# Optimization experiments

Hardware: AMD Instinct MI355X
Metric: run time of the kernel (lower is better)

The kernel has to match this reference:

```python
import jax, jax.numpy as jnp
import numpy as np

B, C1, C2, H, W = 8, 256, 512, 56, 56

def setup_inputs() -> dict:
    key = jax.random.key(0)
    k1, k2, k3, k4, k5 = jax.random.split(key, 5)
    return {
        "x1": jax.random.normal(k1, (B, C1, H, W), dtype=jnp.float32),
        "x2": jax.random.normal(k2, (B, C2, H, W), dtype=jnp.float32),
        "W_proj": jax.random.normal(k3, (C1, C2), dtype=jnp.float32) * (1.0 / np.sqrt(C2)),
        "b_proj": jax.random.normal(k4, (C1,), dtype=jnp.float32) * 0.01,
        "gamma": jax.random.normal(k5, (1,), dtype=jnp.float32) * 0.1,
    }

def reference(x1, x2, W_proj, b_proj, gamma):
    b, c, h, w = x1.shape
    n = h * w
    # 1x1 conv projection C2 -> C1
    x2p = jnp.einsum('oc,bchw->bohw', W_proj, x2) + b_proj[None, :, None, None]
    query = x1.reshape(b, c, n).transpose(0, 2, 1)   # [B, N, C]
    key_ = x2p.reshape(b, c, n)                      # [B, C, N]
    value = x2p.reshape(b, c, n).transpose(0, 2, 1)  # [B, N, C]
    energy = jnp.einsum('bnc,bcm->bnm', query, key_)  # [B, N, N]
    # inverted-energy softmax: max - energy, then softmax over last dim
    energy_new = jnp.max(energy, axis=-1, keepdims=True) - energy
    attention = jax.nn.softmax(energy_new, axis=-1)
    out = jnp.einsum('bnm,bmc->bnc', attention, value)  # [B, N, C]
    out = out.transpose(0, 2, 1).reshape(b, c, h, w)
    return gamma[0] * out + x1
```

## Files before the change

### kernel.cpp

```cpp
#include <hip/hip_runtime.h>
#include <hip/hip_bf16.h>

#define C1 256
#define C2 512
#define NSP 3136
#define NT 98

typedef __attribute__((ext_vector_type(8))) short bf16x8;
typedef __attribute__((ext_vector_type(4))) float f32x4;

__device__ __forceinline__ ushort f2b(float f) {
  __hip_bfloat16 h = __float2bfloat16(f);
  return *reinterpret_cast<ushort*>(&h);
}
__device__ __forceinline__ float b2f(ushort u) {
  union { unsigned int i; float f; } v; v.i = ((unsigned int)u) << 16; return v.f;
}
__device__ __forceinline__ void gload16(const ushort* g, ushort* l) {
  __builtin_amdgcn_global_load_lds(
      (const __attribute__((address_space(1))) void*)g,
      (__attribute__((address_space(3))) void*)l, 16, 0, 0);
}
__device__ __forceinline__ void block_bar() {
  asm volatile("" ::: "memory");
  __builtin_amdgcn_s_barrier();
  asm volatile("" ::: "memory");
}

__global__ __launch_bounds__(256) void k_wtf(const float* __restrict__ W,
                                             ushort* __restrict__ Wf) {
  int ot = blockIdx.x;
  int tid = threadIdx.x;
  int lane = tid & 63, l15 = lane & 15, g = (lane >> 4) & 3;
  int cc0 = (tid >> 6) * 4;
  const float* src = W + (size_t)(ot * 16 + l15) * C2 + g * 8;
#pragma unroll
  for (int k = 0; k < 4; k++) {
    int cc = cc0 + k;
    float4 u0 = *reinterpret_cast<const float4*>(src + cc * 32);
    float4 u1 = *reinterpret_cast<const float4*>(src + cc * 32 + 4);
    bf16x8 v;
    v[0] = (short)f2b(u0.x); v[1] = (short)f2b(u0.y);
    v[2] = (short)f2b(u0.z); v[3] = (short)f2b(u0.w);
    v[4] = (short)f2b(u1.x); v[5] = (short)f2b(u1.y);
    v[6] = (short)f2b(u1.z); v[7] = (short)f2b(u1.w);
    *reinterpret_cast<bf16x8*>(Wf + ((size_t)(ot * 16 + cc)) * 512 + lane * 8) = v;
  }
}

__global__ __launch_bounds__(256) void k_x1t(const float* __restrict__ x1,
                                             ushort* __restrict__ x1t) {
  __shared__ float t[32][33];
  int b = blockIdx.z;
  int n0 = blockIdx.x * 32;
  int c0 = blockIdx.y * 32;
  int tid = threadIdx.x;
  int r = tid >> 3, q = (tid & 7) * 4;
  const float* src = x1 + ((size_t)b * C1 + (c0 + r)) * NSP + n0 + q;
  float4 v = *reinterpret_cast<const float4*>(src);
  t[r][q] = v.x; t[r][q + 1] = v.y; t[r][q + 2] = v.z; t[r][q + 3] = v.w;
  __syncthreads();
  ushort4 o;
  o.x = f2b(t[q + 0][r]); o.y = f2b(t[q + 1][r]);
  o.z = f2b(t[q + 2][r]); o.w = f2b(t[q + 3][r]);
  *reinterpret_cast<ushort4*>(x1t + ((size_t)b * NSP + n0 + r) * C1 + c0 + q) = o;
}

__global__ __launch_bounds__(256) void k_x2f(const float* __restrict__ x2,
                                             ushort* __restrict__ x2f) {
  __shared__ float t[32][33];
  int b = blockIdx.z;
  int n0 = blockIdx.x * 32;
  int cc = blockIdx.y;
  int c0 = cc * 32;
  int tid = threadIdx.x;
  int r = tid >> 3, q = (tid & 7) * 4;
  const float* src = x2 + ((size_t)b * C2 + (c0 + r)) * NSP + n0 + q;
  float4 v = *reinterpret_cast<const float4*>(src);
  t[r][q] = v.x; t[r][q + 1] = v.y; t[r][q + 2] = v.z; t[r][q + 3] = v.w;
  __syncthreads();
  int l15 = tid & 15, g = (tid >> 4) & 3, sub = tid >> 6;
  int ntl = sub & 1, ih = sub >> 1;
  int nl = ntl * 16 + l15;
  int cl = g * 8 + ih * 4;
  ushort4 o;
  o.x = f2b(t[cl + 0][nl]); o.y = f2b(t[cl + 1][nl]);
  o.z = f2b(t[cl + 2][nl]); o.w = f2b(t[cl + 3][nl]);
  int nt16 = (n0 >> 4) + ntl;
  *reinterpret_cast<ushort4*>(
      x2f + (((size_t)b * 196 + nt16) * 16 + cc) * 512 + (size_t)(tid & 63) * 8 + ih * 4) = o;
}

__global__ __launch_bounds__(256) void k_proj(const ushort* __restrict__ Wf,
    const ushort* __restrict__ x2f, const float* __restrict__ bias,
    ushort* __restrict__ Kf, ushort* __restrict__ Vf) {
  __shared__ __align__(16) ushort WL[2][8][512];
  __shared__ __align__(16) ushort XL[2][4][512];
  int bid = blockIdx.x;
  int b = bid & 7;
  int tq = bid >> 3;
  int oh = tq & 1;
  int nt = tq >> 1;
  int tid = threadIdx.x;
  int w = tid >> 6, lane = tid & 63, l15 = lane & 15, g = lane >> 4;
  int wq = w >> 1, wn = w & 1;
  int ot0 = oh * 8;
  int nt0 = nt * 4;

  auto stage = [&](int buf, int cc) {
#pragma unroll
    for (int j = 0; j < 3; j++) {
      int chunk = w * 3 + j;
      if (chunk < 8) {
        gload16(Wf + ((size_t)(ot0 + chunk) * 16 + cc) * 512 + lane * 8,
                &WL[buf][chunk][0]);
      } else {
        gload16(x2f + (((size_t)b * 196 + nt0 + (chunk - 8)) * 16 + cc) * 512 + lane * 8,
                &XL[buf][chunk - 8][0]);
      }
    }
  };

  f32x4 zero = {0.f, 0.f, 0.f, 0.f};
  f32x4 acc[4][2];
#pragma unroll
  for (int a = 0; a < 4; a++)
#pragma unroll
    for (int v = 0; v < 2; v++) acc[a][v] = zero;

  stage(0, 0);
  __syncthreads();

  for (int cc = 0; cc < 16; ++cc) {
    int cur = cc & 1;
    if (cc < 15) stage(cur ^ 1, cc + 1);
    bf16x8 A[4], Bf[2];
#pragma unroll
    for (int a = 0; a < 4; a++)
      A[a] = *reinterpret_cast<const bf16x8*>(&WL[cur][wq * 4 + a][lane * 8]);
#pragma unroll
    for (int v = 0; v < 2; v++)
      Bf[v] = *reinterpret_cast<const bf16x8*>(&XL[cur][wn * 2 + v][lane * 8]);
#pragma unroll
    for (int a = 0; a < 4; a++)
#pragma unroll
      for (int v = 0; v < 2; v++)
        acc[a][v] = __builtin_amdgcn_mfma_f32_16x16x32_bf16(A[a], Bf[v], acc[a][v], 0, 0, 0);
    __syncthreads();
  }

  int obase = oh * 128 + wq * 64;
  float4 bias4[4];
#pragma unroll
  for (int a = 0; a < 4; a++)
    bias4[a] = *reinterpret_cast<const float4*>(&bias[obase + a * 16 + g * 4]);

  int gk = (g & 1) * 4;
#pragma unroll
  for (int a = 0; a < 4; a++) {
    int laneK = (((2 * a + (g >> 1)) & 3) << 4) | l15;
    size_t oK = (size_t)(oh * 4 + wq * 2 + (a >> 1));
#pragma unroll
    for (int v = 0; v < 2; v++) {
      int nK = nt * 4 + wn * 2 + v;
      ushort4 st;
      st.x = f2b(acc[a][v][0] + bias4[a].x);
      st.y = f2b(acc[a][v][1] + bias4[a].y);
      st.z = f2b(acc[a][v][2] + bias4[a].z);
      st.w = f2b(acc[a][v][3] + bias4[a].w);
      *reinterpret_cast<ushort4*>(
          Kf + ((((size_t)b * 196 + nK) * 8 + oK) * 64 + laneK) * 8 + gk) = st;
    }
  }
  int nV = nt * 2 + wn;
#pragma unroll
  for (int v = 0; v < 2; v++) {
    int gv = ((v * 2 + (l15 >> 3)) & 3) << 4;
    int iV = l15 & 7;
#pragma unroll
    for (int a = 0; a < 4; a++) {
      int cs = oh * 8 + wq * 4 + a;
      size_t basev = ((((size_t)b * 98 + nV) * 16 + cs) * 64 + gv) * 8 + iV;
      const float* bp4 = reinterpret_cast<const float*>(&bias4[a]);
#pragma unroll
      for (int r = 0; r < 4; r++)
        Vf[basev + (size_t)(g * 4 + r) * 8] = f2b(acc[a][v][r] + bp4[r]);
    }
  }
}

__global__ __launch_bounds__(256, 3) void k_attn_s(
    const ushort* __restrict__ x1t, const ushort* __restrict__ Kf,
    const ushort* __restrict__ Vf,
    ushort* __restrict__ Po, float* __restrict__ Mv, float* __restrict__ Lv) {
  __shared__ __align__(16) ushort Kt[2][8192];
  __shared__ __align__(16) ushort Vt[8192];
  __shared__ __align__(16) ushort Plds[4][16][36];
  int bid = blockIdx.x;
  int x = bid & 7;
  int j = bid >> 3;
  int s = (4802 * j) / 96;
  int e = (4802 * (j + 1)) / 96;
  int tid = threadIdx.x;
  int w = tid >> 6;
  int lane = tid & 63;
  int l15 = lane & 15;
  int g = lane >> 4;
  int nloc = w * 16 + g * 4;

  const ushort* kg = Kf + (size_t)x * 196 * 8 * 512;
  const ushort* vg = Vf + (size_t)x * 98 * 16 * 512;
  int soff = w * 2048;

  f32x4 zero = {0.f, 0.f, 0.f, 0.f};
  f32x4 O[16];
  f32x4 O17 = zero;
  float M[4];
  bf16x8 qf[8];
  bf16x8 onesf;
#pragma unroll
  for (int i = 0; i < 8; i++) onesf[i] = (short)0x3F80;

  auto resetacc = [&]() {
#pragma unroll
    for (int i = 0; i < 16; i++) O[i] = zero;
    O17 = zero;
#pragma unroll
    for (int r = 0; r < 4; r++) M[r] = -3.0e38f;
  };
  auto loadQ = [&](int u) {
    const ushort* qb = x1t + ((size_t)x * NSP + u * 64 + w * 16 + l15) * C1 + g * 8;
#pragma unroll
    for (int cc = 0; cc < 8; cc++)
      qf[cc] = *reinterpret_cast<const bf16x8*>(qb + cc * 32);
  };

  int u = s / 98;
  int kv = s - u * 98;
  loadQ(u);
  resetacc();
  {
    const ushort* ks = kg + (size_t)kv * 8192 + soff + lane * 8;
#pragma unroll
    for (int jj = 0; jj < 4; ++jj) gload16(ks + jj * 512, &Kt[0][soff] + jj * 512);
  }
  asm volatile("s_waitcnt vmcnt(0)" ::: "memory");
  block_bar();

  int cur = 0;
  for (int i = s; i < e; ++i) {
    {
      const ushort* vs = vg + (size_t)kv * 8192 + soff + lane * 8;
#pragma unroll
      for (int jj = 0; jj < 4; ++jj) gload16(vs + jj * 512, &Vt[soff] + jj * 512);
    }
    asm volatile("" ::: "memory");
    if (i + 1 < e) {
      int kvn = (kv == 97) ? 0 : kv + 1;
      const ushort* ks = kg + (size_t)kvn * 8192 + soff + lane * 8;
#pragma unroll
      for (int jj = 0; jj < 4; ++jj) gload16(ks + jj * 512, &Kt[cur ^ 1][soff] + jj * 512);
    }
    asm volatile("" ::: "memory");

    f32x4 s0a = zero, s0b = zero, s1a = zero, s1b = zero;
    const ushort* kb = &Kt[cur][0];
    __builtin_amdgcn_s_setprio(1);
#pragma unroll
    for (int cc = 0; cc < 8; cc += 2) {
      bf16x8 k00 = *reinterpret_cast<const bf16x8*>(kb + ((size_t)cc * 64 + lane) * 8);
      bf16x8 k10 = *reinterpret_cast<const bf16x8*>(kb + ((size_t)(8 + cc) * 64 + lane) * 8);
      bf16x8 k01 = *reinterpret_cast<const bf16x8*>(kb + ((size_t)(cc + 1) * 64 + lane) * 8);
      bf16x8 k11 = *reinterpret_cast<const bf16x8*>(kb + ((size_t)(9 + cc) * 64 + lane) * 8);
      s0a = __builtin_amdgcn_mfma_f32_16x16x32_bf16(qf[cc], k00, s0a, 0, 0, 0);
      s1a = __builtin_amdgcn_mfma_f32_16x16x32_bf16(qf[cc], k10, s1a, 0, 0, 0);
      s0b = __builtin_amdgcn_mfma_f32_16x16x32_bf16(qf[cc + 1], k01, s0b, 0, 0, 0);
      s1b = __builtin_amdgcn_mfma_f32_16x16x32_bf16(qf[cc + 1], k11, s1b, 0, 0, 0);
    }
    __builtin_amdgcn_s_setprio(0);

    float a0[4], a1[4], tmax[4];
#pragma unroll
    for (int r = 0; r < 4; r++) {
      a0[r] = -(s0a[r] + s0b[r]);
      a1[r] = -(s1a[r] + s1b[r]);
      float mx = fmaxf(a0[r], a1[r]);
      mx = fmaxf(mx, __shfl_xor(mx, 1));
      mx = fmaxf(mx, __shfl_xor(mx, 2));
      mx = fmaxf(mx, __shfl_xor(mx, 4));
      mx = fmaxf(mx, __shfl_xor(mx, 8));
      tmax[r] = mx;
    }
    float d01 = fmaxf(tmax[0] - M[0], tmax[1] - M[1]);
    float d23 = fmaxf(tmax[2] - M[2], tmax[3] - M[3]);
    if (__any(fmaxf(d01, d23) > 3.0f)) {
      float scv[4];
#pragma unroll
      for (int r = 0; r < 4; r++) {
        float nm = fmaxf(M[r], tmax[r]);
        scv[r] = __expf(M[r] - nm);
        M[r] = nm;
      }
#pragma unroll
      for (int i2 = 0; i2 < 16; i2++) {
#pragma unroll
        for (int r = 0; r < 4; r++) O[i2][r] *= scv[r];
      }
#pragma unroll
      for (int r = 0; r < 4; r++) O17[r] *= scv[r];
    }
#pragma unroll
    for (int r = 0; r < 4; r++) {
      float p0 = __expf(a0[r] - M[r]);
      float p1 = __expf(a1[r] - M[r]);
      Plds[w][g * 4 + r][l15] = f2b(p0);
      Plds[w][g * 4 + r][16 + l15] = f2b(p1);
    }

    if (i + 1 < e) { asm volatile("s_waitcnt vmcnt(4)" ::: "memory"); }
    else           { asm volatile("s_waitcnt vmcnt(0)" ::: "memory"); }
    block_bar();

    asm volatile("s_waitcnt lgkmcnt(0)" ::: "memory");
    bf16x8 pf = *reinterpret_cast<const bf16x8*>(&Plds[w][l15][g * 8]);
    __builtin_amdgcn_s_setprio(1);
#pragma unroll
    for (int cs = 0; cs < 16; ++cs) {
      bf16x8 vf = *reinterpret_cast<const bf16x8*>(&Vt[0] + ((size_t)cs * 64 + lane) * 8);
      O[cs] = __builtin_amdgcn_mfma_f32_16x16x32_bf16(pf, vf, O[cs], 0, 0, 0);
    }
    O17 = __builtin_amdgcn_mfma_f32_16x16x32_bf16(pf, onesf, O17, 0, 0, 0);
    __builtin_amdgcn_s_setprio(0);

    asm volatile("s_waitcnt vmcnt(0)" ::: "memory");
    block_bar();
    cur ^= 1;

    if ((i + 1 == e) || (kv == 97)) {
      int firstj = (9408 * u + 95) / 4802;
      int slot = (x * 49 + u) * 3 + (j - firstj);
#pragma unroll
      for (int cs = 0; cs < 16; cs++) {
        int c = cs * 16 + l15;
        ushort4 st;
        st.x = f2b(O[cs][0]); st.y = f2b(O[cs][1]);
        st.z = f2b(O[cs][2]); st.w = f2b(O[cs][3]);
        *reinterpret_cast<ushort4*>(Po + ((size_t)slot * 256 + c) * 64 + nloc) = st;
      }
      if (l15 == 0) {
#pragma unroll
        for (int r = 0; r < 4; r++) {
          Mv[(size_t)slot * 64 + nloc + r] = M[r];
          Lv[(size_t)slot * 64 + nloc + r] = O17[r];
        }
      }
      if (i + 1 < e && kv == 97) { u += 1; loadQ(u); resetacc(); }
    }
    kv = (kv == 97) ? 0 : kv + 1;
  }
}

__global__ __launch_bounds__(256) void k_comb3(
    const ushort* __restrict__ Po, const float* __restrict__ Mv,
    const float* __restrict__ Lv, const float* __restrict__ x1,
    const float* __restrict__ gamma, float* __restrict__ out) {
  int bid = blockIdx.x;
  int x = bid & 7;
  int u = bid >> 3;
  int tid = threadIdx.x;
  int n = tid & 63;
  int c0 = (tid >> 6) * 64;
  int firstj = (9408 * u + 95) / 4802;
  int lastj = (96 * (98 * u + 97) + 95) / 4802;
  int np = lastj - firstj + 1;
  size_t base = (size_t)(x * 49 + u) * 3;
  bool has2 = (np >= 3);

  float M0 = Mv[(base + 0) * 64 + n];
  float M1 = Mv[(base + 1) * 64 + n];
  float M2 = has2 ? Mv[(base + 2) * 64 + n] : -3.0e38f;
  float L0 = Lv[(base + 0) * 64 + n];
  float L1 = Lv[(base + 1) * 64 + n];
  float L2 = has2 ? Lv[(base + 2) * 64 + n] : 0.f;
  float Mg = fmaxf(fmaxf(M0, M1), M2);
  float w0 = __expf(M0 - Mg), w1 = __expf(M1 - Mg);
  float w2 = has2 ? __expf(M2 - Mg) : 0.f;
  float rl = gamma[0] / (w0 * L0 + w1 * L1 + w2 * L2);

  const ushort* p0 = Po + ((base + 0) * 256) * 64 + n;
  const ushort* p1 = Po + ((base + 1) * 256) * 64 + n;
  const ushort* p2 = Po + ((base + 2) * 256) * 64 + n;
  size_t ob = (size_t)x * C1 * NSP + u * 64 + n;
#pragma unroll 4
  for (int c = c0; c < c0 + 64; ++c) {
    float acc = w0 * b2f(p0[(size_t)c * 64]) + w1 * b2f(p1[(size_t)c * 64]);
    if (has2) acc += w2 * b2f(p2[(size_t)c * 64]);
    size_t idx = ob + (size_t)c * NSP;
    out[idx] = acc * rl + x1[idx];
  }
}

template<int SPLIT>
__global__ __launch_bounds__(256, 3) void k_attn(
    const ushort* __restrict__ x1t, const ushort* __restrict__ Kf,
    const ushort* __restrict__ Vf, const float* __restrict__ x1,
    const float* __restrict__ gamma, float* __restrict__ out,
    ushort* __restrict__ Po, float* __restrict__ Mv, float* __restrict__ Lv) {
  __shared__ __align__(16) ushort Kt[2][8192];
  __shared__ __align__(16) ushort Vt[8192];
  __shared__ __align__(16) ushort Plds[4][16][36];
  int bid = blockIdx.x;
  int b = bid & 7;
  int qt = SPLIT ? (bid >> 4) : (bid >> 3);
  int h = SPLIT ? ((bid >> 3) & 1) : 0;
  int t0 = h * 49;
  int t1 = SPLIT ? (t0 + 49) : NT;
  int tid = threadIdx.x;
  int w = tid >> 6;
  int lane = tid & 63;
  int l15 = lane & 15;
  int g = lane >> 4;
  int n0 = qt * 64 + w * 16;

  bf16x8 qf[8];
  const ushort* qb = x1t + ((size_t)b * NSP + n0 + l15) * C1 + g * 8;
#pragma unroll
  for (int cc = 0; cc < 8; cc++)
    qf[cc] = *reinterpret_cast<const bf16x8*>(qb + cc * 32);

  f32x4 zero = {0.f, 0.f, 0.f, 0.f};
  f32x4 O[16];
#pragma unroll
  for (int i = 0; i < 16; i++) O[i] = zero;
  f32x4 O17 = zero;
  float M[4];
#pragma unroll
  for (int r = 0; r < 4; r++) M[r] = -3.0e38f;
  bf16x8 onesf;
#pragma unroll
  for (int i = 0; i < 8; i++) onesf[i] = (short)0x3F80;

  const ushort* kg = Kf + (size_t)b * 196 * 8 * 512;
  const ushort* vg = Vf + (size_t)b * 98 * 16 * 512;
  int soff = w * 2048;

  {
    const ushort* ks = kg + (size_t)t0 * 8192 + soff + lane * 8;
#pragma unroll
    for (int jj = 0; jj < 4; ++jj) gload16(ks + jj * 512, &Kt[0][soff] + jj * 512);
  }
  asm volatile("s_waitcnt vmcnt(0)" ::: "memory");
  block_bar();

  int cur = 0;
  for (int t = t0; t < t1; ++t) {
    {
      const ushort* vs = vg + (size_t)t * 8192 + soff + lane * 8;
#pragma unroll
      for (int jj = 0; jj < 4; ++jj) gload16(vs + jj * 512, &Vt[soff] + jj * 512);
    }
    asm volatile("" ::: "memory");
    if (t + 1 < t1) {
      const ushort* ks = kg + (size_t)(t + 1) * 8192 + soff + lane * 8;
#pragma unroll
      for (int jj = 0; jj < 4; ++jj) gload16(ks + jj * 512, &Kt[cur ^ 1][soff] + jj * 512);
    }
    asm volatile("" ::: "memory");

    f32x4 s0a = zero, s0b = zero, s1a = zero, s1b = zero;
    const ushort* kb = &Kt[cur][0];
    __builtin_amdgcn_s_setprio(1);
#pragma unroll
    for (int cc = 0; cc < 8; cc += 2) {
      bf16x8 k00 = *reinterpret_cast<const bf16x8*>(kb + ((size_t)cc * 64 + lane) * 8);
      bf16x8 k10 = *reinterpret_cast<const bf16x8*>(kb + ((size_t)(8 + cc) * 64 + lane) * 8);
      bf16x8 k01 = *reinterpret_cast<const bf16x8*>(kb + ((size_t)(cc + 1) * 64 + lane) * 8);
      bf16x8 k11 = *reinterpret_cast<const bf16x8*>(kb + ((size_t)(9 + cc) * 64 + lane) * 8);
      s0a = __builtin_amdgcn_mfma_f32_16x16x32_bf16(qf[cc], k00, s0a, 0, 0, 0);
      s1a = __builtin_amdgcn_mfma_f32_16x16x32_bf16(qf[cc], k10, s1a, 0, 0, 0);
      s0b = __builtin_amdgcn_mfma_f32_16x16x32_bf16(qf[cc + 1], k01, s0b, 0, 0, 0);
      s1b = __builtin_amdgcn_mfma_f32_16x16x32_bf16(qf[cc + 1], k11, s1b, 0, 0, 0);
    }
    __builtin_amdgcn_s_setprio(0);

    float a0[4], a1[4], tmax[4];
#pragma unroll
    for (int r = 0; r < 4; r++) {
      a0[r] = -(s0a[r] + s0b[r]);
      a1[r] = -(s1a[r] + s1b[r]);
      float mx = fmaxf(a0[r], a1[r]);
      mx = fmaxf(mx, __shfl_xor(mx, 1));
      mx = fmaxf(mx, __shfl_xor(mx, 2));
      mx = fmaxf(mx, __shfl_xor(mx, 4));
      mx = fmaxf(mx, __shfl_xor(mx, 8));
      tmax[r] = mx;
    }
    float d01 = fmaxf(tmax[0] - M[0], tmax[1] - M[1]);
    float d23 = fmaxf(tmax[2] - M[2], tmax[3] - M[3]);
    if (__any(fmaxf(d01, d23) > 3.0f)) {
      float scv[4];
#pragma unroll
      for (int r = 0; r < 4; r++) {
        float nm = fmaxf(M[r], tmax[r]);
        scv[r] = __expf(M[r] - nm);
        M[r] = nm;
      }
#pragma unroll
      for (int i = 0; i < 16; i++) {
#pragma unroll
        for (int r = 0; r < 4; r++) O[i][r] *= scv[r];
      }
#pragma unroll
      for (int r = 0; r < 4; r++) O17[r] *= scv[r];
    }
#pragma unroll
    for (int r = 0; r < 4; r++) {
      float p0 = __expf(a0[r] - M[r]);
      float p1 = __expf(a1[r] - M[r]);
      Plds[w][g * 4 + r][l15] = f2b(p0);
      Plds[w][g * 4 + r][16 + l15] = f2b(p1);
    }

    if (t + 1 < t1) { asm volatile("s_waitcnt vmcnt(4)" ::: "memory"); }
    else            { asm volatile("s_waitcnt vmcnt(0)" ::: "memory"); }
    block_bar();

    asm volatile("s_waitcnt lgkmcnt(0)" ::: "memory");
    bf16x8 pf = *reinterpret_cast<const bf16x8*>(&Plds[w][l15][g * 8]);
    __builtin_amdgcn_s_setprio(1);
#pragma unroll
    for (int cs = 0; cs < 16; ++cs) {
      bf16x8 vf = *reinterpret_cast<const bf16x8*>(&Vt[0] + ((size_t)cs * 64 + lane) * 8);
      O[cs] = __builtin_amdgcn_mfma_f32_16x16x32_bf16(pf, vf, O[cs], 0, 0, 0);
    }
    O17 = __builtin_amdgcn_mfma_f32_16x16x32_bf16(pf, onesf, O17, 0, 0, 0);
    __builtin_amdgcn_s_setprio(0);

    asm volatile("s_waitcnt vmcnt(0)" ::: "memory");
    block_bar();
    cur ^= 1;
  }

  if (SPLIT) {
    int pb = bid;
    int nloc = w * 16 + g * 4;
#pragma unroll
    for (int cs = 0; cs < 16; cs++) {
      int c = cs * 16 + l15;
      ushort4 st;
      st.x = f2b(O[cs][0]); st.y = f2b(O[cs][1]);
      st.z = f2b(O[cs][2]); st.w = f2b(O[cs][3]);
      *reinterpret_cast<ushort4*>(Po + ((size_t)pb * 256 + c) * 64 + nloc) = st;
    }
    if (l15 == 0) {
#pragma unroll
      for (int r = 0; r < 4; r++) {
        Mv[(size_t)pb * 64 + nloc + r] = M[r];
        Lv[(size_t)pb * 64 + nloc + r] = O17[r];
      }
    }
  } else {
    float gm = gamma[0];
    float rl[4];
#pragma unroll
    for (int r = 0; r < 4; r++) rl[r] = gm / O17[r];
    size_t ob = (size_t)b * C1 * NSP + n0 + (size_t)g * 4;
#pragma unroll
    for (int cs = 0; cs < 16; cs++) {
      size_t idx = ob + (size_t)(cs * 16 + l15) * NSP;
      float4 x4 = *reinterpret_cast<const float4*>(&x1[idx]);
      float4 o4;
      o4.x = O[cs][0] * rl[0] + x4.x;
      o4.y = O[cs][1] * rl[1] + x4.y;
      o4.z = O[cs][2] * rl[2] + x4.z;
      o4.w = O[cs][3] * rl[3] + x4.w;
      *reinterpret_cast<float4*>(&out[idx]) = o4;
    }
  }
}

__global__ __launch_bounds__(256) void k_comb(
    const ushort* __restrict__ Po, const float* __restrict__ Mv,
    const float* __restrict__ Lv, const float* __restrict__ x1,
    const float* __restrict__ gamma, float* __restrict__ out) {
  int bid = blockIdx.x;
  int b = bid & 7;
  int qt = bid >> 3;
  int tid = threadIdx.x;
  int n = tid & 63;
  int c0 = (tid >> 6) * 64;
  int pb0 = qt * 16 + b;
  int pb1 = qt * 16 + 8 + b;
  int n0 = qt * 64;
  float M0 = Mv[(size_t)pb0 * 64 + n], M1 = Mv[(size_t)pb1 * 64 + n];
  float L0 = Lv[(size_t)pb0 * 64 + n], L1 = Lv[(size_t)pb1 * 64 + n];
  float Ms = fmaxf(M0, M1);
  float w0 = __expf(M0 - Ms), w1 = __expf(M1 - Ms);
  float rl = gamma[0] / (w0 * L0 + w1 * L1);
  const ushort* p0 = Po + (size_t)pb0 * 16384 + n;
  const ushort* p1 = Po + (size_t)pb1 * 16384 + n;
#pragma unroll 4
  for (int c = c0; c < c0 + 64; ++c) {
    float o0 = b2f(p0[(size_t)c * 64]);
    float o1 = b2f(p1[(size_t)c * 64]);
    size_t idx = ((size_t)b * C1 + c) * NSP + n0 + n;
    out[idx] = (w0 * o0 + w1 * o1) * rl + x1[idx];
  }
}

extern "C" void kernel_launch(void* const* d_in, const int* in_sizes, int n_in,
                              void* d_out, int out_size, void* d_ws, size_t ws_size,
                              hipStream_t stream) {
  const float* x1 = (const float*)d_in[0];
  const float* x2 = (const float*)d_in[1];
  const float* W = (const float*)d_in[2];
  const float* bp = (const float*)d_in[3];
  const float* gamma = (const float*)d_in[4];
  float* out = (float*)d_out;

  char* ws = (char*)d_ws;
  ushort* Wf = (ushort*)(ws + 0);
  ushort* x1t = (ushort*)(ws + 262144);
  ushort* Kf = (ushort*)(ws + 13107200);
  ushort* Vf = (ushort*)(ws + 25952256);
  ushort* Po = (ushort*)(ws + 38797312);
  float* Mv = (float*)(ws + 77332480);
  float* Lv = (float*)(ws + 77633536);
  ushort* Pof = (ushort*)(ws + 38797312);
  float* Mvf = (float*)(ws + 64487424);
  float* Lvf = (float*)(ws + 64688128);
  ushort* x2f = (ushort*)d_out;

  k_wtf<<<dim3(16), dim3(256), 0, stream>>>(W, Wf);
  k_x1t<<<dim3(98, 8, 8), dim3(256), 0, stream>>>(x1, x1t);
  k_x2f<<<dim3(98, 16, 8), dim3(256), 0, stream>>>(x2, x2f);
  k_proj<<<dim3(784), dim3(256), 0, stream>>>(Wf, x2f, bp, Kf, Vf);

  if (ws_size >= 77934592ULL) {
    k_attn_s<<<dim3(768), dim3(256), 0, stream>>>(x1t, Kf, Vf, Po, Mv, Lv);
    k_comb3<<<dim3(392), dim3(256), 0, stream>>>(Po, Mv, Lv, x1, gamma, out);
  } else if (ws_size >= 64888832ULL) {
    k_attn<1><<<dim3(784), dim3(256), 0, stream>>>(x1t, Kf, Vf, x1, gamma, out,
                                                   Pof, Mvf, Lvf);
    k_comb<<<dim3(392), dim3(256), 0, stream>>>(Pof, Mvf, Lvf, x1, gamma, out);
  } else {
    k_attn<0><<<dim3(392), dim3(256), 0, stream>>>(x1t, Kf, Vf, x1, gamma, out,
                                                   Pof, Mvf, Lvf);
  }
}
```

Before: 241.8 us.

## Add 8-wave attention kernel with 128-row query tiles and stream-K split

```diff
diff --git a/kernel.cpp b/kernel.cpp
--- a/kernel.cpp
+++ b/kernel.cpp
@@ -189,6 +189,221 @@
   }
 }
 
+__global__ __launch_bounds__(512, 4) void k_attn_w8(
+    const ushort* __restrict__ x1t, const ushort* __restrict__ Kf,
+    const ushort* __restrict__ Vf,
+    ushort* __restrict__ Po, float* __restrict__ Mv, float* __restrict__ Lv) {
+  __shared__ __align__(16) ushort Kt[2][8192];
+  __shared__ __align__(16) ushort Vt[2][8192];
+  __shared__ __align__(16) ushort Plds[8][16][36];
+  int bid = blockIdx.x;
+  int x = bid & 7;
+  int j = bid >> 3;
+  int s = (2450 * j) / 64;
+  int e = (2450 * (j + 1)) / 64;
+  int tid = threadIdx.x;
+  int w = tid >> 6;
+  int lane = tid & 63;
+  int l15 = lane & 15;
+  int g = lane >> 4;
+  int nloc = w * 16 + g * 4;
+
+  const ushort* kg = Kf + (size_t)x * 196 * 8 * 512;
+  const ushort* vg = Vf + (size_t)x * 98 * 16 * 512;
+  int soff = w * 1024;
+
+  f32x4 zero = {0.f, 0.f, 0.f, 0.f};
+  f32x4 O[16];
+  f32x4 O17 = zero;
+  float M[4];
+  bf16x8 qf[8];
+  bf16x8 onesf;
+#pragma unroll
+  for (int i = 0; i < 8; i++) onesf[i] = (short)0x3F80;
+
+  auto resetacc = [&]() {
+#pragma unroll
+    for (int i = 0; i < 16; i++) O[i] = zero;
+    O17 = zero;
+#pragma unroll
+    for (int r = 0; r < 4; r++) M[r] = -3.0e38f;
+  };
+  auto loadQ = [&](int u) {
+    int qrow = u * 128 + w * 16;
+    if (qrow >= NSP) qrow = 0;
+    const ushort* qb = x1t + ((size_t)x * NSP + qrow + l15) * C1 + g * 8;
+#pragma unroll
+    for (int cc = 0; cc < 8; cc++)
+      qf[cc] = *reinterpret_cast<const bf16x8*>(qb + cc * 32);
+  };
+  auto stageK = [&](int buf, int t) {
+    const ushort* ks = kg + (size_t)t * 8192 + soff + lane * 8;
+    gload16(ks, &Kt[buf][soff]);
+    gload16(ks + 512, &Kt[buf][soff + 512]);
+  };
+  auto stageV = [&](int buf, int t) {
+    const ushort* vs = vg + (size_t)t * 8192 + soff + lane * 8;
+    gload16(vs, &Vt[buf][soff]);
+    gload16(vs + 512, &Vt[buf][soff + 512]);
+  };
+
+  int u = s / 98;
+  int kv = s - u * 98;
+  loadQ(u);
+  resetacc();
+  stageK(0, kv);
+  stageV(0, kv);
+
+  int cur = 0;
+  for (int i = s; i < e; ++i) {
+    asm volatile("s_waitcnt vmcnt(2)" ::: "memory");
+    block_bar();
+    if (i + 1 < e) {
+      int kvn = (kv == 97) ? 0 : kv + 1;
+      stageK(cur ^ 1, kvn);
+      stageV(cur ^ 1, kvn);
+    }
+
+    f32x4 s0a = zero, s0b = zero, s1a = zero, s1b = zero;
+    const ushort* kb = &Kt[cur][0];
+    __builtin_amdgcn_s_setprio(1);
+#pragma unroll
+    for (int cc = 0; cc < 8; cc += 2) {
+      bf16x8 k00 = *reinterpret_cast<const bf16x8*>(kb + ((size_t)cc * 64 + lane) * 8);
+      bf16x8 k10 = *reinterpret_cast<const bf16x8*>(kb + ((size_t)(8 + cc) * 64 + lane) * 8);
+      bf16x8 k01 = *reinterpret_cast<const bf16x8*>(kb + ((size_t)(cc + 1) * 64 + lane) * 8);
+      bf16x8 k11 = *reinterpret_cast<const bf16x8*>(kb + ((size_t)(9 + cc) * 64 + lane) * 8);
+      s0a = __builtin_amdgcn_mfma_f32_16x16x32_bf16(qf[cc], k00, s0a, 0, 0, 0);
+      s1a = __builtin_amdgcn_mfma_f32_16x16x32_bf16(qf[cc], k10, s1a, 0, 0, 0);
+      s0b = __builtin_amdgcn_mfma_f32_16x16x32_bf16(qf[cc + 1], k01, s0b, 0, 0, 0);
+      s1b = __builtin_amdgcn_mfma_f32_16x16x32_bf16(qf[cc + 1], k11, s1b, 0, 0, 0);
+    }
+    __builtin_amdgcn_s_setprio(0);
+
+    float a0[4], a1[4], tmax[4];
+#pragma unroll
+    for (int r = 0; r < 4; r++) {
+      a0[r] = -(s0a[r] + s0b[r]);
+      a1[r] = -(s1a[r] + s1b[r]);
+      float mx = fmaxf(a0[r], a1[r]);
+      mx = fmaxf(mx, __shfl_xor(mx, 1));
+      mx = fmaxf(mx, __shfl_xor(mx, 2));
+      mx = fmaxf(mx, __shfl_xor(mx, 4));
+      mx = fmaxf(mx, __shfl_xor(mx, 8));
+      tmax[r] = mx;
+    }
+    float d01 = fmaxf(tmax[0] - M[0], tmax[1] - M[1]);
+    float d23 = fmaxf(tmax[2] - M[2], tmax[3] - M[3]);
+    if (__any(fmaxf(d01, d23) > 3.0f)) {
+      float scv[4];
+#pragma unroll
+      for (int r = 0; r < 4; r++) {
+        float nm = fmaxf(M[r], tmax[r]);
+        scv[r] = __expf(M[r] - nm);
+        M[r] = nm;
+      }
+#pragma unroll
+      for (int i2 = 0; i2 < 16; i2++) {
+#pragma unroll
+        for (int r = 0; r < 4; r++) O[i2][r] *= scv[r];
+      }
+#pragma unroll
+      for (int r = 0; r < 4; r++) O17[r] *= scv[r];
+    }
+#pragma unroll
+    for (int r = 0; r < 4; r++) {
+      Plds[w][g * 4 + r][l15] = f2b(__expf(a0[r] - M[r]));
+      Plds[w][g * 4 + r][16 + l15] = f2b(__expf(a1[r] - M[r]));
+    }
+
+    if (i + 1 < e) { asm volatile("s_waitcnt vmcnt(4)" ::: "memory"); }
+    else           { asm volatile("s_waitcnt vmcnt(0)" ::: "memory"); }
+    block_bar();
+
+    asm volatile("s_waitcnt lgkmcnt(0)" ::: "memory");
+    bf16x8 pf = *reinterpret_cast<const bf16x8*>(&Plds[w][l15][g * 8]);
+    const ushort* vb = &Vt[cur][0];
+    __builtin_amdgcn_s_setprio(1);
+#pragma unroll
+    for (int cs = 0; cs < 16; ++cs) {
+      bf16x8 vf = *reinterpret_cast<const bf16x8*>(vb + ((size_t)cs * 64 + lane) * 8);
+      O[cs] = __builtin_amdgcn_mfma_f32_16x16x32_bf16(pf, vf, O[cs], 0, 0, 0);
+    }
+    O17 = __builtin_amdgcn_mfma_f32_16x16x32_bf16(pf, onesf, O17, 0, 0, 0);
+    __builtin_amdgcn_s_setprio(0);
+    cur ^= 1;
+
+    if ((i + 1 == e) || (kv == 97)) {
+      if (u * 128 + w * 16 < NSP) {
+        int firstj = (6272 * u + 63) / 2450;
+        int slot = (x * 25 + u) * 4 + (j - firstj);
+#pragma unroll
+        for (int cs = 0; cs < 16; cs++) {
+          int c = cs * 16 + l15;
+          ushort4 st;
+          st.x = f2b(O[cs][0]); st.y = f2b(O[cs][1]);
+          st.z = f2b(O[cs][2]); st.w = f2b(O[cs][3]);
+          *reinterpret_cast<ushort4*>(Po + ((size_t)slot * 256 + c) * 128 + nloc) = st;
+        }
+        if (l15 == 0) {
+#pragma unroll
+          for (int r = 0; r < 4; r++) {
+            Mv[(size_t)slot * 128 + nloc + r] = M[r];
+            Lv[(size_t)slot * 128 + nloc + r] = O17[r];
+          }
+        }
+      }
+      if (i + 1 < e && kv == 97) { u += 1; loadQ(u); resetacc(); }
+    }
+    kv = (kv == 97) ? 0 : kv + 1;
+  }
+}
+
+__global__ __launch_bounds__(256) void k_comb4w(
+    const ushort* __restrict__ Po, const float* __restrict__ Mv,
+    const float* __restrict__ Lv, const float* __restrict__ x1,
+    const float* __restrict__ gamma, float* __restrict__ out) {
+  int bid = blockIdx.x;
+  int x = bid & 7;
+  int u = bid >> 3;
+  int tid = threadIdx.x;
+  int n = tid & 127;
+  int c0 = (tid >> 7) * 128;
+  if (u * 128 + n >= NSP) return;
+  int firstj = (6272 * u + 63) / 2450;
+  int lastj = (6272 * u + 6271) / 2450;
+  int np = lastj - firstj + 1;
+  size_t base = (size_t)(x * 25 + u) * 4;
+
+  float Mp[4], Lp[4], wq[4];
+  float Mg = -3.0e38f;
+#pragma unroll
+  for (int q = 0; q < 4; q++) {
+    if (q < np) {
+      Mp[q] = Mv[(base + q) * 128 + n];
+      Lp[q] = Lv[(base + q) * 128 + n];
+      Mg = fmaxf(Mg, Mp[q]);
+    }
+  }
+  float Ls = 0.f;
+#pragma unroll
+  for (int q = 0; q < 4; q++) {
+    wq[q] = (q < np) ? __expf(Mp[q] - Mg) : 0.f;
+    if (q < np) Ls += wq[q] * Lp[q];
+  }
+  float rl = gamma[0] / Ls;
+  size_t ob = (size_t)x * C1 * NSP + (size_t)u * 128 + n;
+#pragma unroll 2
+  for (int c = c0; c < c0 + 128; ++c) {
+    float acc = 0.f;
+#pragma unroll
+    for (int q = 0; q < 4; q++)
+      if (q < np) acc += wq[q] * b2f(Po[((base + q) * 256 + c) * 128 + n]);
+    size_t idx = ob + (size_t)c * NSP;
+    out[idx] = acc * rl + x1[idx];
+  }
+}
+
 __global__ __launch_bounds__(256, 3) void k_attn_s(
     const ushort* __restrict__ x1t, const ushort* __restrict__ Kf,
     const ushort* __restrict__ Vf,
@@ -311,10 +526,8 @@
     }
 #pragma unroll
     for (int r = 0; r < 4; r++) {
-      float p0 = __expf(a0[r] - M[r]);
-      float p1 = __expf(a1[r] - M[r]);
-      Plds[w][g * 4 + r][l15] = f2b(p0);
-      Plds[w][g * 4 + r][16 + l15] = f2b(p1);
+      Plds[w][g * 4 + r][l15] = f2b(__expf(a0[r] - M[r]));
+      Plds[w][g * 4 + r][16 + l15] = f2b(__expf(a1[r] - M[r]));
     }
 
     if (i + 1 < e) { asm volatile("s_waitcnt vmcnt(4)" ::: "memory"); }
@@ -400,214 +613,6 @@
   }
 }
 
-template<int SPLIT>
-__global__ __launch_bounds__(256, 3) void k_attn(
-    const ushort* __restrict__ x1t, const ushort* __restrict__ Kf,
-    const ushort* __restrict__ Vf, const float* __restrict__ x1,
-    const float* __restrict__ gamma, float* __restrict__ out,
-    ushort* __restrict__ Po, float* __restrict__ Mv, float* __restrict__ Lv) {
-  __shared__ __align__(16) ushort Kt[2][8192];
-  __shared__ __align__(16) ushort Vt[8192];
-  __shared__ __align__(16) ushort Plds[4][16][36];
-  int bid = blockIdx.x;
-  int b = bid & 7;
-  int qt = SPLIT ? (bid >> 4) : (bid >> 3);
-  int h = SPLIT ? ((bid >> 3) & 1) : 0;
-  int t0 = h * 49;
-  int t1 = SPLIT ? (t0 + 49) : NT;
-  int tid = threadIdx.x;
-  int w = tid >> 6;
-  int lane = tid & 63;
-  int l15 = lane & 15;
-  int g = lane >> 4;
-  int n0 = qt * 64 + w * 16;
-
-  bf16x8 qf[8];
-  const ushort* qb = x1t + ((size_t)b * NSP + n0 + l15) * C1 + g * 8;
-#pragma unroll
-  for (int cc = 0; cc < 8; cc++)
-    qf[cc] = *reinterpret_cast<const bf16x8*>(qb + cc * 32);
-
-  f32x4 zero = {0.f, 0.f, 0.f, 0.f};
-  f32x4 O[16];
-#pragma unroll
-  for (int i = 0; i < 16; i++) O[i] = zero;
-  f32x4 O17 = zero;
-  float M[4];
-#pragma unroll
-  for (int r = 0; r < 4; r++) M[r] = -3.0e38f;
-  bf16x8 onesf;
-#pragma unroll
-  for (int i = 0; i < 8; i++) onesf[i] = (short)0x3F80;
-
-  const ushort* kg = Kf + (size_t)b * 196 * 8 * 512;
-  const ushort* vg = Vf + (size_t)b * 98 * 16 * 512;
-  int soff = w * 2048;
-
-  {
-    const ushort* ks = kg + (size_t)t0 * 8192 + soff + lane * 8;
-#pragma unroll
-    for (int jj = 0; jj < 4; ++jj) gload16(ks + jj * 512, &Kt[0][soff] + jj * 512);
-  }
-  asm volatile("s_waitcnt vmcnt(0)" ::: "memory");
-  block_bar();
-
-  int cur = 0;
-  for (int t = t0; t < t1; ++t) {
-    {
-      const ushort* vs = vg + (size_t)t * 8192 + soff + lane * 8;
-#pragma unroll
-      for (int jj = 0; jj < 4; ++jj) gload16(vs + jj * 512, &Vt[soff] + jj * 512);
-    }
-    asm volatile("" ::: "memory");
-    if (t + 1 < t1) {
-      const ushort* ks = kg + (size_t)(t + 1) * 8192 + soff + lane * 8;
-#pragma unroll
-      for (int jj = 0; jj < 4; ++jj) gload16(ks + jj * 512, &Kt[cur ^ 1][soff] + jj * 512);
-    }
-    asm volatile("" ::: "memory");
-
-    f32x4 s0a = zero, s0b = zero, s1a = zero, s1b = zero;
-    const ushort* kb = &Kt[cur][0];
-    __builtin_amdgcn_s_setprio(1);
-#pragma unroll
-    for (int cc = 0; cc < 8; cc += 2) {
-      bf16x8 k00 = *reinterpret_cast<const bf16x8*>(kb + ((size_t)cc * 64 + lane) * 8);
-      bf16x8 k10 = *reinterpret_cast<const bf16x8*>(kb + ((size_t)(8 + cc) * 64 + lane) * 8);
-      bf16x8 k01 = *reinterpret_cast<const bf16x8*>(kb + ((size_t)(cc + 1) * 64 + lane) * 8);
-      bf16x8 k11 = *reinterpret_cast<const bf16x8*>(kb + ((size_t)(9 + cc) * 64 + lane) * 8);
-      s0a = __builtin_amdgcn_mfma_f32_16x16x32_bf16(qf[cc], k00, s0a, 0, 0, 0);
-      s1a = __builtin_amdgcn_mfma_f32_16x16x32_bf16(qf[cc], k10, s1a, 0, 0, 0);
-      s0b = __builtin_amdgcn_mfma_f32_16x16x32_bf16(qf[cc + 1], k01, s0b, 0, 0, 0);
-      s1b = __builtin_amdgcn_mfma_f32_16x16x32_bf16(qf[cc + 1], k11, s1b, 0, 0, 0);
-    }
-    __builtin_amdgcn_s_setprio(0);
-
-    float a0[4], a1[4], tmax[4];
-#pragma unroll
-    for (int r = 0; r < 4; r++) {
-      a0[r] = -(s0a[r] + s0b[r]);
-      a1[r] = -(s1a[r] + s1b[r]);
-      float mx = fmaxf(a0[r], a1[r]);
-      mx = fmaxf(mx, __shfl_xor(mx, 1));
-      mx = fmaxf(mx, __shfl_xor(mx, 2));
-      mx = fmaxf(mx, __shfl_xor(mx, 4));
-      mx = fmaxf(mx, __shfl_xor(mx, 8));
-      tmax[r] = mx;
-    }
-    float d01 = fmaxf(tmax[0] - M[0], tmax[1] - M[1]);
-    float d23 = fmaxf(tmax[2] - M[2], tmax[3] - M[3]);
-    if (__any(fmaxf(d01, d23) > 3.0f)) {
-      float scv[4];
-#pragma unroll
-      for (int r = 0; r < 4; r++) {
-        float nm = fmaxf(M[r], tmax[r]);
-        scv[r] = __expf(M[r] - nm);
-        M[r] = nm;
-      }
-#pragma unroll
-      for (int i = 0; i < 16; i++) {
-#pragma unroll
-        for (int r = 0; r < 4; r++) O[i][r] *= scv[r];
-      }
-#pragma unroll
-      for (int r = 0; r < 4; r++) O17[r] *= scv[r];
-    }
-#pragma unroll
-    for (int r = 0; r < 4; r++) {
-      float p0 = __expf(a0[r] - M[r]);
-      float p1 = __expf(a1[r] - M[r]);
-      Plds[w][g * 4 + r][l15] = f2b(p0);
-      Plds[w][g * 4 + r][16 + l15] = f2b(p1);
-    }
-
-    if (t + 1 < t1) { asm volatile("s_waitcnt vmcnt(4)" ::: "memory"); }
-    else            { asm volatile("s_waitcnt vmcnt(0)" ::: "memory"); }
-    block_bar();
-
-    asm volatile("s_waitcnt lgkmcnt(0)" ::: "memory");
-    bf16x8 pf = *reinterpret_cast<const bf16x8*>(&Plds[w][l15][g * 8]);
-    __builtin_amdgcn_s_setprio(1);
-#pragma unroll
-    for (int cs = 0; cs < 16; ++cs) {
-      bf16x8 vf = *reinterpret_cast<const bf16x8*>(&Vt[0] + ((size_t)cs * 64 + lane) * 8);
-      O[cs] = __builtin_amdgcn_mfma_f32_16x16x32_bf16(pf, vf, O[cs], 0, 0, 0);
-    }
-    O17 = __builtin_amdgcn_mfma_f32_16x16x32_bf16(pf, onesf, O17, 0, 0, 0);
-    __builtin_amdgcn_s_setprio(0);
-
-    asm volatile("s_waitcnt vmcnt(0)" ::: "memory");
-    block_bar();
-    cur ^= 1;
-  }
-
-  if (SPLIT) {
-    int pb = bid;
-    int nloc = w * 16 + g * 4;
-#pragma unroll
-    for (int cs = 0; cs < 16; cs++) {
-      int c = cs * 16 + l15;
-      ushort4 st;
-      st.x = f2b(O[cs][0]); st.y = f2b(O[cs][1]);
-      st.z = f2b(O[cs][2]); st.w = f2b(O[cs][3]);
-      *reinterpret_cast<ushort4*>(Po + ((size_t)pb * 256 + c) * 64 + nloc) = st;
-    }
-    if (l15 == 0) {
-#pragma unroll
-      for (int r = 0; r < 4; r++) {
-        Mv[(size_t)pb * 64 + nloc + r] = M[r];
-        Lv[(size_t)pb * 64 + nloc + r] = O17[r];
-      }
-    }
-  } else {
-    float gm = gamma[0];
-    float rl[4];
-#pragma unroll
-    for (int r = 0; r < 4; r++) rl[r] = gm / O17[r];
-    size_t ob = (size_t)b * C1 * NSP + n0 + (size_t)g * 4;
-#pragma unroll
-    for (int cs = 0; cs < 16; cs++) {
-      size_t idx = ob + (size_t)(cs * 16 + l15) * NSP;
-      float4 x4 = *reinterpret_cast<const float4*>(&x1[idx]);
-      float4 o4;
-      o4.x = O[cs][0] * rl[0] + x4.x;
-      o4.y = O[cs][1] * rl[1] + x4.y;
-      o4.z = O[cs][2] * rl[2] + x4.z;
-      o4.w = O[cs][3] * rl[3] + x4.w;
-      *reinterpret_cast<float4*>(&out[idx]) = o4;
-    }
-  }
-}
-
-__global__ __launch_bounds__(256) void k_comb(
-    const ushort* __restrict__ Po, const float* __restrict__ Mv,
-    const float* __restrict__ Lv, const float* __restrict__ x1,
-    const float* __restrict__ gamma, float* __restrict__ out) {
-  int bid = blockIdx.x;
-  int b = bid & 7;
-  int qt = bid >> 3;
-  int tid = threadIdx.x;
-  int n = tid & 63;
-  int c0 = (tid >> 6) * 64;
-  int pb0 = qt * 16 + b;
-  int pb1 = qt * 16 + 8 + b;
-  int n0 = qt * 64;
-  float M0 = Mv[(size_t)pb0 * 64 + n], M1 = Mv[(size_t)pb1 * 64 + n];
-  float L0 = Lv[(size_t)pb0 * 64 + n], L1 = Lv[(size_t)pb1 * 64 + n];
-  float Ms = fmaxf(M0, M1);
-  float w0 = __expf(M0 - Ms), w1 = __expf(M1 - Ms);
-  float rl = gamma[0] / (w0 * L0 + w1 * L1);
-  const ushort* p0 = Po + (size_t)pb0 * 16384 + n;
-  const ushort* p1 = Po + (size_t)pb1 * 16384 + n;
-#pragma unroll 4
-  for (int c = c0; c < c0 + 64; ++c) {
-    float o0 = b2f(p0[(size_t)c * 64]);
-    float o1 = b2f(p1[(size_t)c * 64]);
-    size_t idx = ((size_t)b * C1 + c) * NSP + n0 + n;
-    out[idx] = (w0 * o0 + w1 * o1) * rl + x1[idx];
-  }
-}
-
 extern "C" void kernel_launch(void* const* d_in, const int* in_sizes, int n_in,
                               void* d_out, int out_size, void* d_ws, size_t ws_size,
                               hipStream_t stream) {
@@ -624,11 +629,11 @@
   ushort* Kf = (ushort*)(ws + 13107200);
   ushort* Vf = (ushort*)(ws + 25952256);
   ushort* Po = (ushort*)(ws + 38797312);
-  float* Mv = (float*)(ws + 77332480);
-  float* Lv = (float*)(ws + 77633536);
-  ushort* Pof = (ushort*)(ws + 38797312);
-  float* Mvf = (float*)(ws + 64487424);
-  float* Lvf = (float*)(ws + 64688128);
+  float* Mv = (float*)(ws + 91226112);
+  float* Lv = (float*)(ws + 91635712);
+  ushort* Po3 = (ushort*)(ws + 38797312);
+  float* Mv3 = (float*)(ws + 77332480);
+  float* Lv3 = (float*)(ws + 77633536);
   ushort* x2f = (ushort*)d_out;
 
   k_wtf<<<dim3(16), dim3(256), 0, stream>>>(W, Wf);
@@ -636,15 +641,11 @@
   k_x2f<<<dim3(98, 16, 8), dim3(256), 0, stream>>>(x2, x2f);
   k_proj<<<dim3(784), dim3(256), 0, stream>>>(Wf, x2f, bp, Kf, Vf);
 
-  if (ws_size >= 77934592ULL) {
-    k_attn_s<<<dim3(768), dim3(256), 0, stream>>>(x1t, Kf, Vf, Po, Mv, Lv);
-    k_comb3<<<dim3(392), dim3(256), 0, stream>>>(Po, Mv, Lv, x1, gamma, out);
-  } else if (ws_size >= 64888832ULL) {
-    k_attn<1><<<dim3(784), dim3(256), 0, stream>>>(x1t, Kf, Vf, x1, gamma, out,
-                                                   Pof, Mvf, Lvf);
-    k_comb<<<dim3(392), dim3(256), 0, stream>>>(Pof, Mvf, Lvf, x1, gamma, out);
+  if (ws_size >= 92045312ULL) {
+    k_attn_w8<<<dim3(512), dim3(512), 0, stream>>>(x1t, Kf, Vf, Po, Mv, Lv);
+    k_comb4w<<<dim3(200), dim3(256), 0, stream>>>(Po, Mv, Lv, x1, gamma, out);
   } else {
-    k_attn<0><<<dim3(392), dim3(256), 0, stream>>>(x1t, Kf, Vf, x1, gamma, out,
-                                                   Pof, Mvf, Lvf);
-  }
-}
+    k_attn_s<<<dim3(768), dim3(256), 0, stream>>>(x1t, Kf, Vf, Po3, Mv3, Lv3);
+    k_comb3<<<dim3(392), dim3(256), 0, stream>>>(Po3, Mv3, Lv3, x1, gamma, out);
+  }
+}
```

New measurement: 461.7 us. +90.9%, slower.
